# Kernel optimization log

Hardware: AMD Instinct MI355X
Metric: run time of the kernel (lower is better)

Reference implementation:

```python
import jax, jax.numpy as jnp
import numpy as np
from jax.ops import segment_sum


def gcn_conv(x, src, dst, W, b, num_nodes):
    # PyG GCNConv: x' = D^{-1/2} (A + I) D^{-1/2} (x @ W) + b
    loops = jnp.arange(num_nodes, dtype=src.dtype)
    s = jnp.concatenate([src, loops])  # source of each edge (incl. self-loops)
    d = jnp.concatenate([dst, loops])  # destination of each edge
    ones = jnp.ones(s.shape[0], dtype=x.dtype)
    deg = segment_sum(ones, d, num_segments=num_nodes)  # in-degree incl. self-loop
    dinv = jnp.where(deg > 0, jax.lax.rsqrt(deg), 0.0)
    norm = dinv[s] * dinv[d]  # [E+N]
    h = x @ W  # [N, C_out] dense transform first (C_out <= C_in typical)
    msg = h[s] * norm[:, None]  # gather + scale  [E+N, C_out]
    out = segment_sum(msg, d, num_segments=num_nodes)  # scatter-add
    return out + b


def setup_inputs() -> dict:
    key = jax.random.key(0)
    k1, k2, k3, k4 = jax.random.split(key, 4)
    N, E = 100000, 1600000
    C_in, C_out = 64, 32
    C_hid = 2 * C_out
    x = jax.random.normal(k1, (N, C_in), dtype=jnp.float32)
    edge_index = jax.random.randint(k2, (2, E), 0, N, dtype=jnp.int64)
    # Glorot-style init for the linear weights, zero bias (PyG defaults)
    W1 = jax.random.normal(k3, (C_in, C_hid), dtype=jnp.float32) * (1.0 / np.sqrt(C_in))
    b1 = jnp.zeros((C_hid,), dtype=jnp.float32)
    W2 = jax.random.normal(k4, (C_hid, C_out), dtype=jnp.float32) * (1.0 / np.sqrt(C_hid))
    b2 = jnp.zeros((C_out,), dtype=jnp.float32)
    return {"x": x, "edge_index": edge_index, "num_nodes": N,
            "W1": W1, "b1": b1, "W2": W2, "b2": b2}


def reference(x, edge_index, num_nodes, W1, b1, W2, b2):
    src, dst = edge_index[0], edge_index[1]
    h = gcn_conv(x, src, dst, W1, b1, num_nodes)
    h = jax.nn.relu(h)
    out = gcn_conv(h, src, dst, W2, b2, num_nodes)
    return out
```

## Files before the change

### kernel.cpp

```cpp
#include <hip/hip_runtime.h>


constexpr int CAP = 8192;
constexpr int NBMAX = 512;

__device__ inline unsigned short f2bf(float f) {
    unsigned u = __float_as_uint(f);
    u += 0x7fff + ((u >> 16) & 1);
    return (unsigned short)(u >> 16);
}
__device__ inline float bflo(unsigned u) { return __uint_as_float(u << 16); }
__device__ inline float bfhi(unsigned u) { return __uint_as_float(u & 0xffff0000u); }

__global__ __launch_bounds__(256) void p1_bin(const int* __restrict__ src,
                                              const int* __restrict__ dst,
                                              int* __restrict__ bucketCursor,
                                              unsigned* __restrict__ staging, int E, int NB) {
    __shared__ int cnt[NBMAX];
    __shared__ int cur[NBMAX];
    int tid = threadIdx.x;
    for (int i = tid; i < NB; i += 256) cnt[i] = 0;
    __syncthreads();
    int e0 = blockIdx.x * 4096;
#pragma unroll
    for (int k = 0; k < 16; ++k) {
        int e = e0 + k * 256 + tid;
        if (e < E) atomicAdd(&cnt[dst[e] >> 8], 1);
    }
    __syncthreads();
    for (int i = tid; i < NB; i += 256) {
        int c = cnt[i];
        cur[i] = c ? atomicAdd(&bucketCursor[i], c) : 0;
    }
    __syncthreads();
#pragma unroll
    for (int k = 0; k < 16; ++k) {
        int e = e0 + k * 256 + tid;
        if (e < E) {
            int d = dst[e];
            int b = d >> 8;
            int slot = atomicAdd(&cur[b], 1);
            staging[(size_t)b * CAP + slot] = ((unsigned)src[e] << 8) | (unsigned)(d & 255);
        }
    }
}

__global__ __launch_bounds__(256) void p2_csr(const unsigned* __restrict__ staging,
                                              const int* __restrict__ bucketCursor,
                                              int* __restrict__ rp, int* __restrict__ col,
                                              float* __restrict__ dinv, int N, int E, int NB) {
    __shared__ int sb[NBMAX];
    __shared__ int deg[256];
    __shared__ int scn[256];
    __shared__ int cur[256];
    int b = blockIdx.x;
    int tid = threadIdx.x;
    int i1 = tid, i2 = tid + 256;
    sb[i1] = (i1 < NB) ? bucketCursor[i1] : 0;
    sb[i2] = (i2 < NB) ? bucketCursor[i2] : 0;
    deg[tid] = 0;
    __syncthreads();
    for (int off = 1; off < NBMAX; off <<= 1) {
        int a = (i1 >= off) ? sb[i1 - off] : 0;
        int c = (i2 >= off) ? sb[i2 - off] : 0;
        __syncthreads();
        sb[i1] += a;
        sb[i2] += c;
        __syncthreads();
    }
    int base = (b == 0) ? 0 : sb[b - 1];
    int size = sb[b] - base;
    if (b == 0 && tid == 0) rp[N] = E;
    const unsigned* st = staging + (size_t)b * CAP;
    for (int i = tid; i < size; i += 256) atomicAdd(&deg[st[i] & 255u], 1);
    __syncthreads();
    int g = b * 256 + tid;
    int d = deg[tid];
    if (g < N) dinv[g] = rsqrtf((float)(d + 1));
    scn[tid] = d;
    __syncthreads();
    for (int off = 1; off < 256; off <<= 1) {
        int t = (tid >= off) ? scn[tid - off] : 0;
        __syncthreads();
        scn[tid] += t;
        __syncthreads();
    }
    int excl = scn[tid] - d;
    if (g < N) rp[g] = base + excl;
    cur[tid] = excl;
    __syncthreads();
    for (int i = tid; i < size; i += 256) {
        unsigned pk = st[i];
        int pos = atomicAdd(&cur[pk & 255u], 1);
        col[base + pos] = (int)(pk >> 8);
    }
}

__global__ __launch_bounds__(256) void gemm1(const float* __restrict__ X,
                                             const float* __restrict__ W,
                                             const float* __restrict__ dinv,
                                             unsigned short* __restrict__ Hout, int N) {
    constexpr int XS = 65;
    __shared__ float Xs[128 * XS];
    __shared__ float Ws[64 * 64];
    int tid = threadIdx.x;
    int rowBase = blockIdx.x * 128;
    const float4* Wv = (const float4*)W;
    float4* Wsv = (float4*)Ws;
    for (int i = tid; i < 64 * 64 / 4; i += 256) Wsv[i] = Wv[i];
    const float4* Xv = (const float4*)X;
    for (int v = tid; v < 128 * 16; v += 256) {
        int r = v >> 4, j = v & 15;
        int gr = rowBase + r;
        float4 t = make_float4(0.f, 0.f, 0.f, 0.f);
        if (gr < N) t = Xv[(size_t)gr * 16 + j];
        int b = r * XS + j * 4;
        Xs[b] = t.x;
        Xs[b + 1] = t.y;
        Xs[b + 2] = t.z;
        Xs[b + 3] = t.w;
    }
    __syncthreads();
    int cg = tid % 8, rg = tid / 8;
    int c0 = cg * 8, r0 = rg * 4;
    float acc[4][8];
#pragma unroll
    for (int i = 0; i < 4; ++i)
#pragma unroll
        for (int j = 0; j < 8; ++j) acc[i][j] = 0.f;
#pragma unroll 8
    for (int k = 0; k < 64; ++k) {
        float4 w0 = *(const float4*)&Ws[k * 64 + c0];
        float4 w1 = *(const float4*)&Ws[k * 64 + c0 + 4];
        float xr[4];
#pragma unroll
        for (int i = 0; i < 4; ++i) xr[i] = Xs[(r0 + i) * XS + k];
#pragma unroll
        for (int i = 0; i < 4; ++i) {
            acc[i][0] = fmaf(xr[i], w0.x, acc[i][0]);
            acc[i][1] = fmaf(xr[i], w0.y, acc[i][1]);
            acc[i][2] = fmaf(xr[i], w0.z, acc[i][2]);
            acc[i][3] = fmaf(xr[i], w0.w, acc[i][3]);
            acc[i][4] = fmaf(xr[i], w1.x, acc[i][4]);
            acc[i][5] = fmaf(xr[i], w1.y, acc[i][5]);
            acc[i][6] = fmaf(xr[i], w1.z, acc[i][6]);
            acc[i][7] = fmaf(xr[i], w1.w, acc[i][7]);
        }
    }
#pragma unroll
    for (int i = 0; i < 4; ++i) {
        int row = rowBase + r0 + i;
        if (row >= N) continue;
        float dn = dinv[row];
        unsigned pk[4];
#pragma unroll
        for (int j = 0; j < 4; ++j) {
            unsigned lo = f2bf(acc[i][2 * j] * dn);
            unsigned hi = f2bf(acc[i][2 * j + 1] * dn);
            pk[j] = lo | (hi << 16);
        }
        *(uint4*)(Hout + (size_t)row * 64 + c0) = make_uint4(pk[0], pk[1], pk[2], pk[3]);
    }
}

__global__ __launch_bounds__(256) void agg1_gemm2(
    const uint4* __restrict__ hs1, const float* __restrict__ dinv, const int* __restrict__ rp,
    const int* __restrict__ col, const float* __restrict__ b1, const float* __restrict__ W2,
    unsigned short* __restrict__ h2, int N) {
    constexpr int RS = 68;
    constexpr int NPB = 64;
    __shared__ float rows[NPB * RS];
    __shared__ float Ws2[64 * 32];
    __shared__ int ctr;
    int tid = threadIdx.x;
    const float4* W2v = (const float4*)W2;
    float4* Ws2v = (float4*)Ws2;
    for (int i = tid; i < 64 * 32 / 4; i += 256) Ws2v[i] = W2v[i];
    if (tid == 0) ctr = 32;
    __syncthreads();

    int lane = tid & 63;
    int gbase = lane & ~7;
    int q = tid & 7;
    int cur = tid >> 3;
    int blockBase = blockIdx.x * NPB;
    while (cur < NPB) {
        int node = blockBase + cur;
        if (node < N) {
            float dn = dinv[node];
            float acc[8];
            uint4 u = hs1[(size_t)node * 8 + q];
            acc[0] = bflo(u.x); acc[1] = bfhi(u.x);
            acc[2] = bflo(u.y); acc[3] = bfhi(u.y);
            acc[4] = bflo(u.z); acc[5] = bfhi(u.z);
            acc[6] = bflo(u.w); acc[7] = bfhi(u.w);
            int e0 = rp[node], e1 = rp[node + 1];
            int e = e0;
#define ACC8(U)                               \
    acc[0] += bflo(U.x); acc[1] += bfhi(U.x); \
    acc[2] += bflo(U.y); acc[3] += bfhi(U.y); \
    acc[4] += bflo(U.z); acc[5] += bfhi(U.z); \
    acc[6] += bflo(U.w); acc[7] += bfhi(U.w);
            for (; e + 4 <= e1; e += 4) {
                int s0 = col[e], s1 = col[e + 1], s2 = col[e + 2], s3 = col[e + 3];
                uint4 u0 = hs1[(size_t)s0 * 8 + q];
                uint4 u1 = hs1[(size_t)s1 * 8 + q];
                uint4 u2 = hs1[(size_t)s2 * 8 + q];
                uint4 u3 = hs1[(size_t)s3 * 8 + q];
                ACC8(u0) ACC8(u1) ACC8(u2) ACC8(u3)
            }
            for (; e < e1; ++e) {
                uint4 uu = hs1[(size_t)col[e] * 8 + q];
                ACC8(uu)
            }
#undef ACC8
            const float4* bv = (const float4*)b1;
            float4 bb0 = bv[q * 2], bb1 = bv[q * 2 + 1];
            float* myrow = &rows[cur * RS + q * 8];
            *(float4*)myrow =
                make_float4(fmaxf(fmaf(acc[0], dn, bb0.x), 0.f), fmaxf(fmaf(acc[1], dn, bb0.y), 0.f),
                            fmaxf(fmaf(acc[2], dn, bb0.z), 0.f), fmaxf(fmaf(acc[3], dn, bb0.w), 0.f));
            *(float4*)(myrow + 4) =
                make_float4(fmaxf(fmaf(acc[4], dn, bb1.x), 0.f), fmaxf(fmaf(acc[5], dn, bb1.y), 0.f),
                            fmaxf(fmaf(acc[6], dn, bb1.z), 0.f), fmaxf(fmaf(acc[7], dn, bb1.w), 0.f));
        }
        int nxt = 0;
        if (q == 0) nxt = atomicAdd(&ctr, 1);
        nxt = __shfl(nxt, gbase, 64);
        cur = nxt;
    }
    __syncthreads();

    int r = tid >> 2;
    int c0 = (tid & 3) * 8;
    int node = blockBase + r;
    if (node >= N) return;
    float dn = dinv[node];
    float acc2[8];
#pragma unroll
    for (int j = 0; j < 8; ++j) acc2[j] = 0.f;
    const float* row = &rows[r * RS];
#pragma unroll
    for (int k4 = 0; k4 < 16; ++k4) {
        float4 xq = *(const float4*)&row[k4 * 4];
#pragma unroll
        for (int kk = 0; kk < 4; ++kk) {
            float xv = (&xq.x)[kk];
            float4 wa = *(const float4*)&Ws2[(k4 * 4 + kk) * 32 + c0];
            float4 wb = *(const float4*)&Ws2[(k4 * 4 + kk) * 32 + c0 + 4];
            acc2[0] = fmaf(xv, wa.x, acc2[0]);
            acc2[1] = fmaf(xv, wa.y, acc2[1]);
            acc2[2] = fmaf(xv, wa.z, acc2[2]);
            acc2[3] = fmaf(xv, wa.w, acc2[3]);
            acc2[4] = fmaf(xv, wb.x, acc2[4]);
            acc2[5] = fmaf(xv, wb.y, acc2[5]);
            acc2[6] = fmaf(xv, wb.z, acc2[6]);
            acc2[7] = fmaf(xv, wb.w, acc2[7]);
        }
    }
    unsigned pk[4];
#pragma unroll
    for (int j = 0; j < 4; ++j) {
        unsigned lo = f2bf(acc2[2 * j] * dn);
        unsigned hi = f2bf(acc2[2 * j + 1] * dn);
        pk[j] = lo | (hi << 16);
    }
    *(uint4*)(h2 + (size_t)node * 32 + c0) = make_uint4(pk[0], pk[1], pk[2], pk[3]);
}

__global__ __launch_bounds__(256) void agg2(const uint4* __restrict__ hs2,
                                            const float* __restrict__ dinv,
                                            const int* __restrict__ rp,
                                            const int* __restrict__ col,
                                            const float* __restrict__ bias,
                                            float* __restrict__ out, int N) {
    constexpr int NPB = 128;
    __shared__ int ctr;
    int tid = threadIdx.x;
    if (tid == 0) ctr = 64;
    __syncthreads();
    int lane = tid & 63;
    int gbase = lane & ~3;
    int q = tid & 3;
    int cur = tid >> 2;
    int blockBase = blockIdx.x * NPB;
    while (cur < NPB) {
        int node = blockBase + cur;
        if (node < N) {
            float acc[8];
            uint4 u = hs2[(size_t)node * 4 + q];
            acc[0] = bflo(u.x); acc[1] = bfhi(u.x);
            acc[2] = bflo(u.y); acc[3] = bfhi(u.y);
            acc[4] = bflo(u.z); acc[5] = bfhi(u.z);
            acc[6] = bflo(u.w); acc[7] = bfhi(u.w);
            int e0 = rp[node], e1 = rp[node + 1];
            int e = e0;
#define ACC8(U)                               \
    acc[0] += bflo(U.x); acc[1] += bfhi(U.x); \
    acc[2] += bflo(U.y); acc[3] += bfhi(U.y); \
    acc[4] += bflo(U.z); acc[5] += bfhi(U.z); \
    acc[6] += bflo(U.w); acc[7] += bfhi(U.w);
            for (; e + 4 <= e1; e += 4) {
                int s0 = col[e], s1 = col[e + 1], s2 = col[e + 2], s3 = col[e + 3];
                uint4 u0 = hs2[(size_t)s0 * 4 + q];
                uint4 u1 = hs2[(size_t)s1 * 4 + q];
                uint4 u2 = hs2[(size_t)s2 * 4 + q];
                uint4 u3 = hs2[(size_t)s3 * 4 + q];
                ACC8(u0) ACC8(u1) ACC8(u2) ACC8(u3)
            }
            for (; e < e1; ++e) {
                uint4 uu = hs2[(size_t)col[e] * 4 + q];
                ACC8(uu)
            }
#undef ACC8
            float dn = dinv[node];
            const float4* bv = (const float4*)bias;
            float4 b0 = bv[q * 2], b1 = bv[q * 2 + 1];
            float4* ov = (float4*)(out + (size_t)node * 32 + q * 8);
            ov[0] = make_float4(fmaf(acc[0], dn, b0.x), fmaf(acc[1], dn, b0.y),
                                fmaf(acc[2], dn, b0.z), fmaf(acc[3], dn, b0.w));
            ov[1] = make_float4(fmaf(acc[4], dn, b1.x), fmaf(acc[5], dn, b1.y),
                                fmaf(acc[6], dn, b1.z), fmaf(acc[7], dn, b1.w));
        }
        int nxt = 0;
        if (q == 0) nxt = atomicAdd(&ctr, 1);
        nxt = __shfl(nxt, gbase, 64);
        cur = nxt;
    }
}

extern "C" void kernel_launch(void* const* d_in, const int* in_sizes, int n_in,
                              void* d_out, int out_size, void* d_ws, size_t ws_size,
                              hipStream_t stream) {
    const float* x = (const float*)d_in[0];
    const int* ei = (const int*)d_in[1];
    const float* W1 = (const float*)d_in[3];
    const float* b1 = (const float*)d_in[4];
    const float* W2 = (const float*)d_in[5];
    const float* b2 = (const float*)d_in[6];

    constexpr int CIN = 64, CHID = 64;
    const int N = in_sizes[0] / CIN;
    const int E = in_sizes[1] / 2;
    const int* src = ei;
    const int* dst = ei + E;
    const int NB = (N + 255) >> 8;

    char* p = (char*)d_ws;
    auto carve = [&](size_t bytes) -> void* {
        void* q = (void*)p;
        p += (bytes + 255) & ~(size_t)255;
        return q;
    };
    int* bucketCursor = (int*)carve((size_t)NB * 4);
    int* rp = (int*)carve((size_t)(N + 1) * 4);
    int* col = (int*)carve((size_t)E * 4);
    float* dinv = (float*)carve((size_t)N * 4);
    unsigned* staging = (unsigned*)carve((size_t)NB * CAP * 4);
    unsigned short* h1 = (unsigned short*)carve((size_t)N * CHID * 2);
    unsigned short* h2 = (unsigned short*)staging;

    hipMemsetAsync(bucketCursor, 0, (size_t)NB * 4, stream);
    p1_bin<<<(E + 4095) / 4096, 256, 0, stream>>>(src, dst, bucketCursor, staging, E, NB);
    p2_csr<<<NB, 256, 0, stream>>>(staging, bucketCursor, rp, col, dinv, N, E, NB);

    gemm1<<<(N + 127) / 128, 256, 0, stream>>>(x, W1, dinv, h1, N);
    agg1_gemm2<<<(N + 63) / 64, 256, 0, stream>>>((const uint4*)h1, dinv, rp, col, b1, W2, h2, N);
    agg2<<<(N + 127) / 128, 256, 0, stream>>>((const uint4*)h2, dinv, rp, col, b2, (float*)d_out,
                                              N);
}
```

Before: 220.2 us.

## Split each node's edge list across two thread groups, drop atomic work queue

Both aggregation kernels now assign two thread subgroups per node, each walking half of the node's CSR edge range, and combine the partial sums with a cross-lane shuffle. The block-local atomic work-stealing loop is removed in favour of a static node-to-thread mapping with smaller blocks (16 nodes per block in agg1_gemm2, 32 per block in agg2). The second GEMM is re-mapped so each thread computes two output columns. The intent is more memory-level parallelism for the gathers and less scheduling overhead, at the cost of more threads and shuffle work and no dynamic load balancing for skewed degrees.

```diff
diff --git a/kernel.cpp b/kernel.cpp
--- a/kernel.cpp
+++ b/kernel.cpp
@@ -163,82 +163,84 @@
     }
 }
 
+#define WALK8(HS, STRIDE)                                                   \
+    {                                                                       \
+        int e = es;                                                         \
+        for (; e + 4 <= ee; e += 4) {                                       \
+            int s0 = col[e], s1 = col[e + 1], s2 = col[e + 2],              \
+                s3 = col[e + 3];                                            \
+            uint4 u0 = HS[(size_t)s0 * STRIDE + q];                         \
+            uint4 u1 = HS[(size_t)s1 * STRIDE + q];                         \
+            uint4 u2 = HS[(size_t)s2 * STRIDE + q];                         \
+            uint4 u3 = HS[(size_t)s3 * STRIDE + q];                         \
+            ACC8(u0) ACC8(u1) ACC8(u2) ACC8(u3)                             \
+        }                                                                   \
+        for (; e < ee; ++e) {                                               \
+            uint4 uu = HS[(size_t)col[e] * STRIDE + q];                     \
+            ACC8(uu)                                                        \
+        }                                                                   \
+    }
+#define ACC8(U)                               \
+    acc[0] += bflo(U.x); acc[1] += bfhi(U.x); \
+    acc[2] += bflo(U.y); acc[3] += bfhi(U.y); \
+    acc[4] += bflo(U.z); acc[5] += bfhi(U.z); \
+    acc[6] += bflo(U.w); acc[7] += bfhi(U.w);
+
 __global__ __launch_bounds__(256) void agg1_gemm2(
     const uint4* __restrict__ hs1, const float* __restrict__ dinv, const int* __restrict__ rp,
     const int* __restrict__ col, const float* __restrict__ b1, const float* __restrict__ W2,
     unsigned short* __restrict__ h2, int N) {
     constexpr int RS = 68;
-    constexpr int NPB = 64;
+    constexpr int NPB = 16;
     __shared__ float rows[NPB * RS];
     __shared__ float Ws2[64 * 32];
-    __shared__ int ctr;
     int tid = threadIdx.x;
     const float4* W2v = (const float4*)W2;
     float4* Ws2v = (float4*)Ws2;
     for (int i = tid; i < 64 * 32 / 4; i += 256) Ws2v[i] = W2v[i];
-    if (tid == 0) ctr = 32;
-    __syncthreads();
-
-    int lane = tid & 63;
-    int gbase = lane & ~7;
-    int q = tid & 7;
-    int cur = tid >> 3;
-    int blockBase = blockIdx.x * NPB;
-    while (cur < NPB) {
-        int node = blockBase + cur;
-        if (node < N) {
-            float dn = dinv[node];
-            float acc[8];
+
+    int r = tid >> 4;
+    int t16 = tid & 15;
+    int sg = t16 >> 3;
+    int q = t16 & 7;
+    int node = blockIdx.x * NPB + r;
+    float dn = 0.f;
+    float acc[8];
+#pragma unroll
+    for (int j = 0; j < 8; ++j) acc[j] = 0.f;
+    if (node < N) {
+        dn = dinv[node];
+        if (sg == 0) {
             uint4 u = hs1[(size_t)node * 8 + q];
             acc[0] = bflo(u.x); acc[1] = bfhi(u.x);
             acc[2] = bflo(u.y); acc[3] = bfhi(u.y);
             acc[4] = bflo(u.z); acc[5] = bfhi(u.z);
             acc[6] = bflo(u.w); acc[7] = bfhi(u.w);
-            int e0 = rp[node], e1 = rp[node + 1];
-            int e = e0;
-#define ACC8(U)                               \
-    acc[0] += bflo(U.x); acc[1] += bfhi(U.x); \
-    acc[2] += bflo(U.y); acc[3] += bfhi(U.y); \
-    acc[4] += bflo(U.z); acc[5] += bfhi(U.z); \
-    acc[6] += bflo(U.w); acc[7] += bfhi(U.w);
-            for (; e + 4 <= e1; e += 4) {
-                int s0 = col[e], s1 = col[e + 1], s2 = col[e + 2], s3 = col[e + 3];
-                uint4 u0 = hs1[(size_t)s0 * 8 + q];
-                uint4 u1 = hs1[(size_t)s1 * 8 + q];
-                uint4 u2 = hs1[(size_t)s2 * 8 + q];
-                uint4 u3 = hs1[(size_t)s3 * 8 + q];
-                ACC8(u0) ACC8(u1) ACC8(u2) ACC8(u3)
-            }
-            for (; e < e1; ++e) {
-                uint4 uu = hs1[(size_t)col[e] * 8 + q];
-                ACC8(uu)
-            }
-#undef ACC8
-            const float4* bv = (const float4*)b1;
-            float4 bb0 = bv[q * 2], bb1 = bv[q * 2 + 1];
-            float* myrow = &rows[cur * RS + q * 8];
-            *(float4*)myrow =
-                make_float4(fmaxf(fmaf(acc[0], dn, bb0.x), 0.f), fmaxf(fmaf(acc[1], dn, bb0.y), 0.f),
-                            fmaxf(fmaf(acc[2], dn, bb0.z), 0.f), fmaxf(fmaf(acc[3], dn, bb0.w), 0.f));
-            *(float4*)(myrow + 4) =
-                make_float4(fmaxf(fmaf(acc[4], dn, bb1.x), 0.f), fmaxf(fmaf(acc[5], dn, bb1.y), 0.f),
-                            fmaxf(fmaf(acc[6], dn, bb1.z), 0.f), fmaxf(fmaf(acc[7], dn, bb1.w), 0.f));
-        }
-        int nxt = 0;
-        if (q == 0) nxt = atomicAdd(&ctr, 1);
-        nxt = __shfl(nxt, gbase, 64);
-        cur = nxt;
-    }
-    __syncthreads();
-
-    int r = tid >> 2;
-    int c0 = (tid & 3) * 8;
-    int node = blockBase + r;
+        }
+        int e0 = rp[node], e1 = rp[node + 1];
+        int mid = (e0 + e1 + 1) >> 1;
+        int es = sg ? mid : e0;
+        int ee = sg ? e1 : mid;
+        WALK8(hs1, 8)
+    }
+#pragma unroll
+    for (int j = 0; j < 8; ++j) acc[j] += __shfl_xor(acc[j], 8, 64);
+    if (node < N && sg == 0) {
+        const float4* bv = (const float4*)b1;
+        float4 bb0 = bv[q * 2], bb1 = bv[q * 2 + 1];
+        float* myrow = &rows[r * RS + q * 8];
+        *(float4*)myrow =
+            make_float4(fmaxf(fmaf(acc[0], dn, bb0.x), 0.f), fmaxf(fmaf(acc[1], dn, bb0.y), 0.f),
+                        fmaxf(fmaf(acc[2], dn, bb0.z), 0.f), fmaxf(fmaf(acc[3], dn, bb0.w), 0.f));
+        *(float4*)(myrow + 4) =
+            make_float4(fmaxf(fmaf(acc[4], dn, bb1.x), 0.f), fmaxf(fmaf(acc[5], dn, bb1.y), 0.f),
+                        fmaxf(fmaf(acc[6], dn, bb1.z), 0.f), fmaxf(fmaf(acc[7], dn, bb1.w), 0.f));
+    }
+    __syncthreads();
+
     if (node >= N) return;
-    float dn = dinv[node];
-    float acc2[8];
-#pragma unroll
-    for (int j = 0; j < 8; ++j) acc2[j] = 0.f;
+    int c0 = t16 * 2;
+    float a0 = 0.f, a1 = 0.f;
     const float* row = &rows[r * RS];
 #pragma unroll
     for (int k4 = 0; k4 < 16; ++k4) {
@@ -246,26 +248,13 @@
 #pragma unroll
         for (int kk = 0; kk < 4; ++kk) {
             float xv = (&xq.x)[kk];
-            float4 wa = *(const float4*)&Ws2[(k4 * 4 + kk) * 32 + c0];
-            float4 wb = *(const float4*)&Ws2[(k4 * 4 + kk) * 32 + c0 + 4];
-            acc2[0] = fmaf(xv, wa.x, acc2[0]);
-            acc2[1] = fmaf(xv, wa.y, acc2[1]);
-            acc2[2] = fmaf(xv, wa.z, acc2[2]);
-            acc2[3] = fmaf(xv, wa.w, acc2[3]);
-            acc2[4] = fmaf(xv, wb.x, acc2[4]);
-            acc2[5] = fmaf(xv, wb.y, acc2[5]);
-            acc2[6] = fmaf(xv, wb.z, acc2[6]);
-            acc2[7] = fmaf(xv, wb.w, acc2[7]);
-        }
-    }
-    unsigned pk[4];
-#pragma unroll
-    for (int j = 0; j < 4; ++j) {
-        unsigned lo = f2bf(acc2[2 * j] * dn);
-        unsigned hi = f2bf(acc2[2 * j + 1] * dn);
-        pk[j] = lo | (hi << 16);
-    }
-    *(uint4*)(h2 + (size_t)node * 32 + c0) = make_uint4(pk[0], pk[1], pk[2], pk[3]);
+            float2 w = *(const float2*)&Ws2[(k4 * 4 + kk) * 32 + c0];
+            a0 = fmaf(xv, w.x, a0);
+            a1 = fmaf(xv, w.y, a1);
+        }
+    }
+    unsigned pk = (unsigned)f2bf(a0 * dn) | ((unsigned)f2bf(a1 * dn) << 16);
+    *(unsigned*)(h2 + (size_t)node * 32 + c0) = pk;
 }
 
 __global__ __launch_bounds__(256) void agg2(const uint4* __restrict__ hs2,
@@ -274,59 +263,37 @@
                                             const int* __restrict__ col,
                                             const float* __restrict__ bias,
                                             float* __restrict__ out, int N) {
-    constexpr int NPB = 128;
-    __shared__ int ctr;
-    int tid = threadIdx.x;
-    if (tid == 0) ctr = 64;
-    __syncthreads();
-    int lane = tid & 63;
-    int gbase = lane & ~3;
-    int q = tid & 3;
-    int cur = tid >> 2;
-    int blockBase = blockIdx.x * NPB;
-    while (cur < NPB) {
-        int node = blockBase + cur;
-        if (node < N) {
-            float acc[8];
-            uint4 u = hs2[(size_t)node * 4 + q];
-            acc[0] = bflo(u.x); acc[1] = bfhi(u.x);
-            acc[2] = bflo(u.y); acc[3] = bfhi(u.y);
-            acc[4] = bflo(u.z); acc[5] = bfhi(u.z);
-            acc[6] = bflo(u.w); acc[7] = bfhi(u.w);
-            int e0 = rp[node], e1 = rp[node + 1];
-            int e = e0;
-#define ACC8(U)                               \
-    acc[0] += bflo(U.x); acc[1] += bfhi(U.x); \
-    acc[2] += bflo(U.y); acc[3] += bfhi(U.y); \
-    acc[4] += bflo(U.z); acc[5] += bfhi(U.z); \
-    acc[6] += bflo(U.w); acc[7] += bfhi(U.w);
-            for (; e + 4 <= e1; e += 4) {
-                int s0 = col[e], s1 = col[e + 1], s2 = col[e + 2], s3 = col[e + 3];
-                uint4 u0 = hs2[(size_t)s0 * 4 + q];
-                uint4 u1 = hs2[(size_t)s1 * 4 + q];
-                uint4 u2 = hs2[(size_t)s2 * 4 + q];
-                uint4 u3 = hs2[(size_t)s3 * 4 + q];
-                ACC8(u0) ACC8(u1) ACC8(u2) ACC8(u3)
-            }
-            for (; e < e1; ++e) {
-                uint4 uu = hs2[(size_t)col[e] * 4 + q];
-                ACC8(uu)
-            }
-#undef ACC8
-            float dn = dinv[node];
-            const float4* bv = (const float4*)bias;
-            float4 b0 = bv[q * 2], b1 = bv[q * 2 + 1];
-            float4* ov = (float4*)(out + (size_t)node * 32 + q * 8);
-            ov[0] = make_float4(fmaf(acc[0], dn, b0.x), fmaf(acc[1], dn, b0.y),
-                                fmaf(acc[2], dn, b0.z), fmaf(acc[3], dn, b0.w));
-            ov[1] = make_float4(fmaf(acc[4], dn, b1.x), fmaf(acc[5], dn, b1.y),
-                                fmaf(acc[6], dn, b1.z), fmaf(acc[7], dn, b1.w));
-        }
-        int nxt = 0;
-        if (q == 0) nxt = atomicAdd(&ctr, 1);
-        nxt = __shfl(nxt, gbase, 64);
-        cur = nxt;
-    }
+    int tid = blockIdx.x * blockDim.x + threadIdx.x;
+    int node = tid >> 3;
+    int t8 = tid & 7;
+    int sg = t8 >> 2, q = t8 & 3;
+    if (node >= N) return;
+    float acc[8];
+#pragma unroll
+    for (int j = 0; j < 8; ++j) acc[j] = 0.f;
+    if (sg == 0) {
+        uint4 u = hs2[(size_t)node * 4 + q];
+        acc[0] = bflo(u.x); acc[1] = bfhi(u.x);
+        acc[2] = bflo(u.y); acc[3] = bfhi(u.y);
+        acc[4] = bflo(u.z); acc[5] = bfhi(u.z);
+        acc[6] = bflo(u.w); acc[7] = bfhi(u.w);
+    }
+    int e0 = rp[node], e1 = rp[node + 1];
+    int mid = (e0 + e1 + 1) >> 1;
+    int es = sg ? mid : e0;
+    int ee = sg ? e1 : mid;
+    WALK8(hs2, 4)
+#pragma unroll
+    for (int j = 0; j < 8; ++j) acc[j] += __shfl_xor(acc[j], 4, 64);
+    if (sg) return;
+    float dn = dinv[node];
+    const float4* bv = (const float4*)bias;
+    float4 b0 = bv[q * 2], b1 = bv[q * 2 + 1];
+    float4* ov = (float4*)(out + (size_t)node * 32 + q * 8);
+    ov[0] = make_float4(fmaf(acc[0], dn, b0.x), fmaf(acc[1], dn, b0.y), fmaf(acc[2], dn, b0.z),
+                        fmaf(acc[3], dn, b0.w));
+    ov[1] = make_float4(fmaf(acc[4], dn, b1.x), fmaf(acc[5], dn, b1.y), fmaf(acc[6], dn, b1.z),
+                        fmaf(acc[7], dn, b1.w));
 }
 
 extern "C" void kernel_launch(void* const* d_in, const int* in_sizes, int n_in,
@@ -365,7 +332,7 @@
     p2_csr<<<NB, 256, 0, stream>>>(staging, bucketCursor, rp, col, dinv, N, E, NB);
 
     gemm1<<<(N + 127) / 128, 256, 0, stream>>>(x, W1, dinv, h1, N);
-    agg1_gemm2<<<(N + 63) / 64, 256, 0, stream>>>((const uint4*)h1, dinv, rp, col, b1, W2, h2, N);
-    agg2<<<(N + 127) / 128, 256, 0, stream>>>((const uint4*)h2, dinv, rp, col, b2, (float*)d_out,
-                                              N);
-}
+    agg1_gemm2<<<(N + 15) / 16, 256, 0, stream>>>((const uint4*)h1, dinv, rp, col, b1, W2, h2, N);
+    agg2<<<((size_t)N * 8 + 255) / 256, 256, 0, stream>>>((const uint4*)h2, dinv, rp, col, b2,
+                                                          (float*)d_out, N);
+}
```

New measurement: 212.6 us. 1.04x faster.
